# Kernel optimization log

Measured on AMD Instinct MI355X. Metric: run time of the kernel, lower is better.

The kernel has to match this reference:

```python
import jax, jax.numpy as jnp
import numpy as np

B, N, D, DE, E, L = 8, 4096, 128, 128, 262144, 2
FF = 4 * D  # feedforward hidden


def _ln(x, g, b, eps=1e-5):
    m = jnp.mean(x, axis=-1, keepdims=True)
    v = jnp.mean(jnp.square(x - m), axis=-1, keepdims=True)
    return (x - m) * jax.lax.rsqrt(v + eps) * g + b


def setup_inputs() -> dict:
    key = jax.random.key(0)
    ks = iter(jax.random.split(key, 40))

    def w(shape):
        fan_in = shape[-2]
        return jax.random.normal(next(ks), shape, jnp.float32) / np.sqrt(fan_in)

    return {
        "x": jax.random.normal(next(ks), (B, N, D), jnp.float32),
        "edge_index": jax.random.randint(next(ks), (2, E), 0, B * N, dtype=jnp.int32),
        "edge_attr": jax.random.normal(next(ks), (E, DE), jnp.float32),
        # message MLP (n_message = 3 linears)
        "msg_W0": w((L, 2 * D + DE, D)), "msg_b0": jnp.zeros((L, D)),
        "msg_W1": w((L, D, D)), "msg_b1": jnp.zeros((L, D)),
        "msg_W2": w((L, D, D)), "msg_b2": jnp.zeros((L, D)),
        "norm0_g": jnp.ones((L, D)), "norm0_b": jnp.zeros((L, D)),
        # feedforward
        "ff_W0": w((L, D, FF)), "ff_b0": jnp.zeros((L, FF)),
        "ff_W1": w((L, FF, D)), "ff_b1": jnp.zeros((L, D)),
        "norm1_g": jnp.ones((L, D)), "norm1_b": jnp.zeros((L, D)),
        # edge update MLP (n_edge_gvps = 3 linears)
        "edge_W0": w((L, 2 * D + DE, DE)), "edge_b0": jnp.zeros((L, DE)),
        "edge_W1": w((L, DE, DE)), "edge_b1": jnp.zeros((L, DE)),
        "edge_W2": w((L, DE, DE)), "edge_b2": jnp.zeros((L, DE)),
        "enorm_g": jnp.ones((L, DE)), "enorm_b": jnp.zeros((L, DE)),
    }


def reference(x, edge_index, edge_attr,
              msg_W0, msg_b0, msg_W1, msg_b1, msg_W2, msg_b2,
              norm0_g, norm0_b, ff_W0, ff_b0, ff_W1, ff_b1, norm1_g, norm1_b,
              edge_W0, edge_b0, edge_W1, edge_b1, edge_W2, edge_b2,
              enorm_g, enorm_b):
    Bx, Nx, Dx = x.shape
    n_nodes = Bx * Nx
    nodes = x.reshape(n_nodes, Dx)          # torch.flatten(x, 0, 1)
    src, dst = edge_index[0], edge_index[1]
    # in-degree for mean aggregation (guard isolated nodes)
    deg = jax.ops.segment_sum(jnp.ones((edge_attr.shape[0],), nodes.dtype), dst,
                              num_segments=n_nodes)
    inv_deg = (1.0 / jnp.maximum(deg, 1.0))[:, None]

    n_layers = msg_W0.shape[0]
    for l in range(n_layers):
        # --- node message passing (mean aggr at dst) ---
        h = jnp.concatenate([nodes[src], edge_attr, nodes[dst]], axis=-1)  # [E, 2D+DE]
        m = jax.nn.relu(h @ msg_W0[l] + msg_b0[l])
        m = jax.nn.relu(m @ msg_W1[l] + msg_b1[l])
        m = m @ msg_W2[l] + msg_b2[l]
        agg = jax.ops.segment_sum(m, dst, num_segments=n_nodes) * inv_deg
        nodes = _ln(nodes + agg, norm0_g[l], norm0_b[l])
        # --- feedforward ---
        ff = jax.nn.relu(nodes @ ff_W0[l] + ff_b0[l]) @ ff_W1[l] + ff_b1[l]
        nodes = _ln(nodes + ff, norm1_g[l], norm1_b[l])
        # --- edge update ---
        eh = jnp.concatenate([nodes[src], edge_attr, nodes[dst]], axis=-1)
        e = jax.nn.relu(eh @ edge_W0[l] + edge_b0[l])
        e = jax.nn.relu(e @ edge_W1[l] + edge_b1[l])
        e = e @ edge_W2[l] + edge_b2[l]
        edge_attr = _ln(edge_attr + e, enorm_g[l], enorm_b[l])

    return nodes.reshape(Bx, Nx, Dx)
```

## Files before the change

kernel.cpp:

```cpp
#include <hip/hip_runtime.h>

#define E_      262144
#define NNODES  32768
#define L_      2

typedef __attribute__((ext_vector_type(8))) short  bf16x8;
typedef __attribute__((ext_vector_type(4))) float  f32x4;

typedef __attribute__((address_space(1))) const unsigned int gu32;
typedef __attribute__((address_space(3))) unsigned int       lu32;

__device__ __forceinline__ void gl16(const void* g, void* l) {
    __builtin_amdgcn_global_load_lds((gu32*)g, (lu32*)l, 16, 0, 0);
}

__device__ __forceinline__ float bf2f(unsigned short u) {
    union { unsigned int i; float f; } v; v.i = ((unsigned int)u) << 16; return v.f;
}
__device__ __forceinline__ unsigned short f2bf(float f) {
    union { float f; unsigned int i; } v; v.f = f;
    unsigned int r = v.i + 0x7FFFu + ((v.i >> 16) & 1u);
    return (unsigned short)(r >> 16);
}

__global__ __launch_bounds__(256)
void k_cvt2(const float* __restrict__ a, unsigned short* __restrict__ oa, int n4a,
            const float* __restrict__ b, unsigned short* __restrict__ ob, int n4b)
{
    int i = blockIdx.x * 256 + threadIdx.x;
    if (i < n4a) {
        float4 v = reinterpret_cast<const float4*>(a)[i];
        ushort4 o; o.x = f2bf(v.x); o.y = f2bf(v.y); o.z = f2bf(v.z); o.w = f2bf(v.w);
        reinterpret_cast<ushort4*>(oa)[i] = o;
    } else if (i < n4a + n4b) {
        int j = i - n4a;
        float4 v = reinterpret_cast<const float4*>(b)[j];
        ushort4 o; o.x = f2bf(v.x); o.y = f2bf(v.y); o.z = f2bf(v.z); o.w = f2bf(v.w);
        reinterpret_cast<ushort4*>(ob)[j] = o;
    }
}

struct TD  { const float* s; unsigned short* d; int off; int K; int nsh; };
struct TDA { TD v[13]; int total; };

__global__ __launch_bounds__(256)
void k_transpose_all(TDA t)
{
    int idx = blockIdx.x * 256 + threadIdx.x;
    if (idx >= t.total) return;
    int j = 0;
#pragma unroll
    for (int m = 1; m < 13; ++m) if (idx >= t.v[m].off) j = m;
    const TD& td = t.v[j];
    int local = idx - td.off;
    int k = local >> td.nsh;
    int n = local & ((1 << td.nsh) - 1);
    td.d[(size_t)n * td.K + k] = f2bf(td.s[local]);
}

template<bool LNEPI>
__global__ __launch_bounds__(256, 4)
void fused_mlp3(const unsigned short* __restrict__ nodes,
                const unsigned short* __restrict__ eattr,
                const int*            __restrict__ ei,
                const unsigned short* __restrict__ W0T,
                const unsigned short* __restrict__ W1T,
                const unsigned short* __restrict__ W2T,
                const float* __restrict__ b0, const float* __restrict__ b1,
                const float* __restrict__ b2,
                const float* __restrict__ g,  const float* __restrict__ bb,
                unsigned short* __restrict__ out)
{
    __shared__ unsigned short S0[64 * 64];
    __shared__ unsigned short SB[128 * 64];
    __shared__ unsigned short H [64 * 128];

    const int tid  = threadIdx.x;
    const int lane = tid & 63;
    const int w    = tid >> 6;
    const int wr   = w >> 1, wc = w & 1;
    const int m0   = blockIdx.x * 64;

    const int lrow = lane >> 3;
    const int soff = ((lane & 7) ^ lrow) * 8;

    char* S0c = (char*)S0;
    char* SBc = (char*)SB;
    char* Hc  = (char*)H;

    const unsigned short *pS[2], *pD[2], *pE[2];
#pragma unroll
    for (int i = 0; i < 2; ++i) {
        int r = w * 16 + i * 8 + lrow;
        int e = m0 + r;
        pS[i] = nodes + (size_t)ei[e]      * 128 + soff;
        pD[i] = nodes + (size_t)ei[E_ + e] * 128 + soff;
        pE[i] = eattr + (size_t)e          * 128 + soff;
    }

    f32x4 acc[2][4];
    auto zacc = [&]() {
#pragma unroll
        for (int m = 0; m < 2; ++m)
#pragma unroll
            for (int n = 0; n < 4; ++n) acc[m][n] = (f32x4){0.f, 0.f, 0.f, 0.f};
    };

    auto mma = [&](const char* Ab, int abytes, int kbase) {
#pragma unroll
        for (int ks = 0; ks < 2; ++ks) {
            const int kb = (kbase + ks * 32) * 2 + (lane >> 4) * 16;
            bf16x8 a[2], b[4];
#pragma unroll
            for (int m = 0; m < 2; ++m) {
                int row = wr * 32 + m * 16 + (lane & 15);
                a[m] = *reinterpret_cast<const bf16x8*>(Ab + row * abytes + (kb ^ ((row & 7) << 4)));
            }
            const int kbb = ks * 64 + (lane >> 4) * 16;
#pragma unroll
            for (int n = 0; n < 4; ++n) {
                int row = wc * 64 + n * 16 + (lane & 15);
                b[n] = *reinterpret_cast<const bf16x8*>(SBc + row * 128 + (kbb ^ ((row & 7) << 4)));
            }
#pragma unroll
            for (int m = 0; m < 2; ++m)
#pragma unroll
                for (int n = 0; n < 4; ++n)
                    acc[m][n] = __builtin_amdgcn_mfma_f32_16x16x32_bf16(a[m], b[n], acc[m][n], 0, 0, 0);
        }
    };

    auto towrite = [&](const float* bias) {
#pragma unroll
        for (int n = 0; n < 4; ++n) {
            int cg = wc * 64 + n * 16 + (lane & 15);
            float bi = bias[cg];
#pragma unroll
            for (int m = 0; m < 2; ++m) {
#pragma unroll
                for (int j = 0; j < 4; ++j) {
                    int rg = wr * 32 + m * 16 + (lane >> 4) * 4 + j;
                    float v = fmaxf(acc[m][n][j] + bi, 0.f);
                    *(unsigned short*)(Hc + rg * 256 + ((2 * cg) ^ ((rg & 7) << 4))) = f2bf(v);
                }
            }
        }
    };

    zacc();
    for (int k0 = 0; k0 < 384; k0 += 64) {
#pragma unroll
        for (int i = 0; i < 2; ++i) {
            const unsigned short* pa = (k0 < 128 ? pS[i] : (k0 < 256 ? pE[i] : pD[i])) + (k0 & 64);
            gl16(pa, S0c + (w * 16 + i * 8) * 128);
        }
#pragma unroll
        for (int i = 0; i < 4; ++i)
            gl16(W0T + (size_t)(w * 32 + i * 8 + lrow) * 384 + k0 + soff,
                 SBc + (w * 32 + i * 8) * 128);
        __syncthreads();
        mma(S0c, 128, 0);
        __syncthreads();
    }
    towrite(b0);
    zacc();
#pragma unroll
    for (int k0 = 0; k0 < 128; k0 += 64) {
#pragma unroll
        for (int i = 0; i < 4; ++i)
            gl16(W1T + (size_t)(w * 32 + i * 8 + lrow) * 128 + k0 + soff,
                 SBc + (w * 32 + i * 8) * 128);
        __syncthreads();
        mma(Hc, 256, k0);
        __syncthreads();
    }
    towrite(b1);
    zacc();
#pragma unroll
    for (int k0 = 0; k0 < 128; k0 += 64) {
#pragma unroll
        for (int i = 0; i < 4; ++i)
            gl16(W2T + (size_t)(w * 32 + i * 8 + lrow) * 128 + k0 + soff,
                 SBc + (w * 32 + i * 8) * 128);
        __syncthreads();
        mma(Hc, 256, k0);
        __syncthreads();
    }

    if (!LNEPI) {
#pragma unroll
        for (int n = 0; n < 4; ++n) {
            int cg = wc * 64 + n * 16 + (lane & 15);
            float bi = b2[cg];
#pragma unroll
            for (int m = 0; m < 2; ++m) {
                int rg = m0 + wr * 32 + m * 16 + (lane >> 4) * 4;
                unsigned short* cp = out + (size_t)rg * 128 + cg;
#pragma unroll
                for (int j = 0; j < 4; ++j)
                    cp[(size_t)j * 128] = f2bf(acc[m][n][j] + bi);
            }
        }
    } else {
#pragma unroll
        for (int n = 0; n < 4; ++n) {
            int cg = wc * 64 + n * 16 + (lane & 15);
            float bi = b2[cg];
#pragma unroll
            for (int m = 0; m < 2; ++m) {
#pragma unroll
                for (int j = 0; j < 4; ++j) {
                    int rg = m0 + wr * 32 + m * 16 + (lane >> 4) * 4 + j;
                    acc[m][n][j] += bi + bf2f(eattr[(size_t)rg * 128 + cg]);
                }
            }
        }
        float* ps = (float*)SBc;
        float* pq = ps + 128;
#pragma unroll
        for (int m = 0; m < 2; ++m) {
#pragma unroll
            for (int j = 0; j < 4; ++j) {
                float s = 0.f, q = 0.f;
#pragma unroll
                for (int n = 0; n < 4; ++n) {
                    float v = acc[m][n][j];
                    s += v; q += v * v;
                }
#pragma unroll
                for (int msk = 1; msk < 16; msk <<= 1) {
                    s += __shfl_xor(s, msk);
                    q += __shfl_xor(q, msk);
                }
                if ((lane & 15) == 0) {
                    int rl = wr * 32 + m * 16 + (lane >> 4) * 4 + j;
                    ps[wc * 64 + rl] = s;
                    pq[wc * 64 + rl] = q;
                }
            }
        }
        __syncthreads();
#pragma unroll
        for (int m = 0; m < 2; ++m) {
#pragma unroll
            for (int j = 0; j < 4; ++j) {
                int rl = wr * 32 + m * 16 + (lane >> 4) * 4 + j;
                float S = ps[rl] + ps[64 + rl];
                float Q = pq[rl] + pq[64 + rl];
                float mean = S * (1.f / 128.f);
                float var  = Q * (1.f / 128.f) - mean * mean;
                float rs   = rsqrtf(var + 1e-5f);
                int rg = m0 + rl;
#pragma unroll
                for (int n = 0; n < 4; ++n) {
                    int cg = wc * 64 + n * 16 + (lane & 15);
                    out[(size_t)rg * 128 + cg] =
                        f2bf((acc[m][n][j] - mean) * rs * g[cg] + bb[cg]);
                }
            }
        }
    }
}

template<int BM, int K, int NTOT, bool RELU>
__global__ __launch_bounds__(256)
void mlp_gemm(const unsigned short* __restrict__ Abase,
              const unsigned short* __restrict__ WT,
              const float*          __restrict__ bias,
              unsigned short*       __restrict__ C)
{
    constexpr int MI = BM / 32;
    __shared__ unsigned short Alds[BM * 64];
    __shared__ unsigned short Blds[128 * 64];

    const int tid  = threadIdx.x;
    const int lane = tid & 63;
    const int w    = tid >> 6;
    const int wr   = w >> 1, wc = w & 1;
    const int m0   = blockIdx.x * BM;
    const int n0   = blockIdx.y * 128;

    const int lrow = lane >> 3;
    const int soff = ((lane & 7) ^ lrow) * 8;

    const unsigned short *pS[MI], *pB[4];
#pragma unroll
    for (int i = 0; i < MI; ++i)
        pS[i] = Abase + (size_t)(m0 + w * (BM / 4) + i * 8 + lrow) * K + soff;
#pragma unroll
    for (int i = 0; i < 4; ++i)
        pB[i] = WT + (size_t)(n0 + w * 32 + i * 8 + lrow) * K + soff;

    f32x4 acc[MI][4];
#pragma unroll
    for (int m = 0; m < MI; ++m)
#pragma unroll
        for (int n = 0; n < 4; ++n) acc[m][n] = (f32x4){0.f, 0.f, 0.f, 0.f};

#pragma unroll
    for (int k0 = 0; k0 < K; k0 += 64) {
#pragma unroll
        for (int i = 0; i < MI; ++i)
            gl16(pS[i] + k0, Alds + (w * (BM / 4) + i * 8) * 64);
#pragma unroll
        for (int i = 0; i < 4; ++i)
            gl16(pB[i] + k0, Blds + (w * 32 + i * 8) * 64);
        __syncthreads();

#pragma unroll
        for (int ks = 0; ks < 2; ++ks) {
            const int kb = ks * 64 + (lane >> 4) * 16;
            bf16x8 a[MI], b[4];
#pragma unroll
            for (int m = 0; m < MI; ++m) {
                int row = wr * (BM / 2) + m * 16 + (lane & 15);
                a[m] = *reinterpret_cast<const bf16x8*>(
                    (const char*)Alds + row * 128 + (kb ^ ((row & 7) << 4)));
            }
#pragma unroll
            for (int n = 0; n < 4; ++n) {
                int row = wc * 64 + n * 16 + (lane & 15);
                b[n] = *reinterpret_cast<const bf16x8*>(
                    (const char*)Blds + row * 128 + (kb ^ ((row & 7) << 4)));
            }
#pragma unroll
            for (int m = 0; m < MI; ++m)
#pragma unroll
                for (int n = 0; n < 4; ++n)
                    acc[m][n] = __builtin_amdgcn_mfma_f32_16x16x32_bf16(a[m], b[n], acc[m][n], 0, 0, 0);
        }
        __syncthreads();
    }

#pragma unroll
    for (int n = 0; n < 4; ++n) {
        int colg = n0 + wc * 64 + n * 16 + (lane & 15);
        float bi = bias[colg];
#pragma unroll
        for (int m = 0; m < MI; ++m) {
            int rowg = m0 + wr * (BM / 2) + m * 16 + (lane >> 4) * 4;
            unsigned short* cp = C + (size_t)rowg * NTOT + colg;
#pragma unroll
            for (int j = 0; j < 4; ++j) {
                float r = acc[m][n][j] + bi;
                if (RELU) r = fmaxf(r, 0.f);
                cp[(size_t)j * NTOT] = f2bf(r);
            }
        }
    }
}

__global__ __launch_bounds__(256)
void k_deg(const int* __restrict__ ei, int* __restrict__ deg)
{
    int e = blockIdx.x * 256 + threadIdx.x;
    atomicAdd(&deg[ei[E_ + e]], 1);
}

__global__ __launch_bounds__(1024)
void k_scan(const int* __restrict__ deg, int* __restrict__ off)
{
    __shared__ int part[1024];
    const int t = threadIdx.x;
    const int base = t * 32;
    int loc[32];
    int s = 0;
#pragma unroll
    for (int i = 0; i < 32; ++i) { loc[i] = s; s += deg[base + i]; }
    part[t] = s;
    __syncthreads();
    for (int d = 1; d < 1024; d <<= 1) {
        int v = (t >= d) ? part[t - d] : 0;
        __syncthreads();
        part[t] += v;
        __syncthreads();
    }
    const int pre = (t == 0) ? 0 : part[t - 1];
#pragma unroll
    for (int i = 0; i < 32; ++i) off[base + i] = pre + loc[i];
    if (t == 1023) off[NNODES] = pre + s;
}

__global__ __launch_bounds__(256)
void k_bucket(const int* __restrict__ ei, int* __restrict__ cursor, int* __restrict__ elist)
{
    int e = blockIdx.x * 256 + threadIdx.x;
    int d = ei[E_ + e];
    int pos = atomicAdd(&cursor[d], 1);
    elist[pos] = e;
}

__global__ __launch_bounds__(256)
void k_aggln(const unsigned short* __restrict__ m,
             const int* __restrict__ off, const int* __restrict__ elist,
             const unsigned short* __restrict__ nodes_in,
             const float* __restrict__ g, const float* __restrict__ bb,
             unsigned short* __restrict__ nodes_out)
{
    const int v    = blockIdx.x * 4 + (threadIdx.x >> 6);
    const int lane = threadIdx.x & 63;
    const int c    = lane * 2;
    const int beg  = off[v], end = off[v + 1];

    float a0 = 0.f, a1 = 0.f;
    for (int i = beg; i < end; ++i) {
        int e = elist[i];
        unsigned int u = *reinterpret_cast<const unsigned int*>(m + (size_t)e * 128 + c);
        a0 += bf2f((unsigned short)(u & 0xffffu));
        a1 += bf2f((unsigned short)(u >> 16));
    }
    const float inv = 1.f / fmaxf((float)(end - beg), 1.f);
    const size_t o = (size_t)v * 128 + c;
    float x0 = bf2f(nodes_in[o])     + a0 * inv;
    float x1 = bf2f(nodes_in[o + 1]) + a1 * inv;

    float s = x0 + x1, sq = x0 * x0 + x1 * x1;
#pragma unroll
    for (int mm = 1; mm < 64; mm <<= 1) { s += __shfl_xor(s, mm); sq += __shfl_xor(sq, mm); }
    float mean = s * (1.f / 128.f);
    float var  = sq * (1.f / 128.f) - mean * mean;
    float rs   = rsqrtf(var + 1e-5f);
    nodes_out[o]     = f2bf((x0 - mean) * rs * g[c]     + bb[c]);
    nodes_out[o + 1] = f2bf((x1 - mean) * rs * g[c + 1] + bb[c + 1]);
}

template<bool F32OUT>
__global__ __launch_bounds__(256)
void k_ln(const unsigned short* __restrict__ base,
          const unsigned short* __restrict__ res,
          const float* __restrict__ g, const float* __restrict__ bb,
          void* __restrict__ outp)
{
    int row  = blockIdx.x * 4 + (threadIdx.x >> 6);
    int lane = threadIdx.x & 63;
    int c    = lane * 2;
    size_t off = (size_t)row * 128 + c;

    float x0 = bf2f(base[off])     + bf2f(res[off]);
    float x1 = bf2f(base[off + 1]) + bf2f(res[off + 1]);
    float s = x0 + x1, sq = x0 * x0 + x1 * x1;
#pragma unroll
    for (int m = 1; m < 64; m <<= 1) { s += __shfl_xor(s, m); sq += __shfl_xor(sq, m); }
    float mean = s * (1.f / 128.f);
    float var  = sq * (1.f / 128.f) - mean * mean;
    float rs   = rsqrtf(var + 1e-5f);
    float y0 = (x0 - mean) * rs * g[c]     + bb[c];
    float y1 = (x1 - mean) * rs * g[c + 1] + bb[c + 1];
    if (F32OUT) {
        ((float*)outp)[off]     = y0;
        ((float*)outp)[off + 1] = y1;
    } else {
        ((unsigned short*)outp)[off]     = f2bf(y0);
        ((unsigned short*)outp)[off + 1] = f2bf(y1);
    }
}

extern "C" void kernel_launch(void* const* d_in, const int* in_sizes, int n_in,
                              void* d_out, int out_size, void* d_ws, size_t ws_size,
                              hipStream_t stream)
{
    const float* x      = (const float*)d_in[0];
    const int*   ei     = (const int*)d_in[1];
    const float* eat0   = (const float*)d_in[2];
    const float* msg_W0 = (const float*)d_in[3];
    const float* msg_b0 = (const float*)d_in[4];
    const float* msg_W1 = (const float*)d_in[5];
    const float* msg_b1 = (const float*)d_in[6];
    const float* msg_W2 = (const float*)d_in[7];
    const float* msg_b2 = (const float*)d_in[8];
    const float* n0g    = (const float*)d_in[9];
    const float* n0b    = (const float*)d_in[10];
    const float* ff_W0  = (const float*)d_in[11];
    const float* ff_b0  = (const float*)d_in[12];
    const float* ff_W1  = (const float*)d_in[13];
    const float* ff_b1  = (const float*)d_in[14];
    const float* n1g    = (const float*)d_in[15];
    const float* n1b    = (const float*)d_in[16];
    const float* e_W0   = (const float*)d_in[17];
    const float* e_b0   = (const float*)d_in[18];
    const float* e_W1   = (const float*)d_in[19];
    const float* e_b1   = (const float*)d_in[20];
    const float* e_W2   = (const float*)d_in[21];
    const float* e_b2   = (const float*)d_in[22];
    const float* eng    = (const float*)d_in[23];
    const float* enb    = (const float*)d_in[24];

    char* ws = (char*)d_ws;
    const size_t MB = (size_t)1 << 20;
    unsigned short* nodes = (unsigned short*)(ws);
    unsigned short* edgec = (unsigned short*)(ws + 8 * MB);
    unsigned short* tmpA  = (unsigned short*)(ws + 72 * MB);
    unsigned short* ffh   = (unsigned short*)(ws + 136 * MB);
    unsigned short* ffo   = tmpA;
    unsigned short* wt    = (unsigned short*)(ws + 200 * MB);
    int*            deg   = (int*)(ws + 202 * MB);
    int*            off   = (int*)(ws + 202 * MB + 256 * 1024);
    int*            cur   = (int*)(ws + 202 * MB + 512 * 1024);
    int*            elist = (int*)(ws + 202 * MB + 768 * 1024);

    unsigned short* p = wt;
    unsigned short *wt_m0[L_], *wt_m1[L_], *wt_m2[L_], *wt_f0[L_], *wt_f1[L_];
    for (int l = 0; l < L_; ++l) {
        wt_m0[l] = p; p += 384 * 128;
        wt_m1[l] = p; p += 128 * 128;
        wt_m2[l] = p; p += 128 * 128;
        wt_f0[l] = p; p += 128 * 512;
        wt_f1[l] = p; p += 512 * 128;
    }
    unsigned short* wt_e0 = p; p += 384 * 128;
    unsigned short* wt_e1 = p; p += 128 * 128;
    unsigned short* wt_e2 = p; p += 128 * 128;

    TDA tda; int toff = 0, ti = 0;
    auto addT = [&](const float* s, unsigned short* d, int K, int N) {
        tda.v[ti++] = TD{s, d, toff, K, (N == 512 ? 9 : 7)};
        toff += K * N;
    };
    for (int l = 0; l < L_; ++l) {
        addT(msg_W0 + l * 384 * 128, wt_m0[l], 384, 128);
        addT(msg_W1 + l * 128 * 128, wt_m1[l], 128, 128);
        addT(msg_W2 + l * 128 * 128, wt_m2[l], 128, 128);
        addT(ff_W0  + l * 128 * 512, wt_f0[l], 128, 512);
        addT(ff_W1  + l * 512 * 128, wt_f1[l], 512, 128);
    }
    addT(e_W0, wt_e0, 384, 128);
    addT(e_W1, wt_e1, 128, 128);
    addT(e_W2, wt_e2, 128, 128);
    tda.total = toff;
    k_transpose_all<<<(toff + 255) / 256, 256, 0, stream>>>(tda);

    const int n4a = NNODES * 128 / 4, n4b = E_ * 128 / 4;
    k_cvt2<<<(n4a + n4b + 255) / 256, 256, 0, stream>>>(x, nodes, n4a, eat0, edgec, n4b);

    hipMemsetAsync(deg, 0, NNODES * sizeof(int), stream);
    k_deg<<<E_ / 256, 256, 0, stream>>>(ei, deg);
    k_scan<<<1, 1024, 0, stream>>>(deg, off);
    hipMemcpyAsync(cur, off, NNODES * sizeof(int), hipMemcpyDeviceToDevice, stream);
    k_bucket<<<E_ / 256, 256, 0, stream>>>(ei, cur, elist);

    const dim3 gE(E_ / 64, 1), gN64(NNODES / 64, 1), gF0(NNODES / 128, 4);

    for (int l = 0; l < L_; ++l) {
        fused_mlp3<false><<<gE, 256, 0, stream>>>(nodes, edgec, ei,
            wt_m0[l], wt_m1[l], wt_m2[l],
            msg_b0 + l * 128, msg_b1 + l * 128, msg_b2 + l * 128,
            nullptr, nullptr, tmpA);
        k_aggln<<<NNODES / 4, 256, 0, stream>>>(tmpA, off, elist, nodes,
            n0g + l * 128, n0b + l * 128, nodes);
        mlp_gemm<128, 128, 512, true ><<<gF0, 256, 0, stream>>>(nodes, wt_f0[l], ff_b0 + l * 512, ffh);
        mlp_gemm<64,  512, 128, false><<<gN64, 256, 0, stream>>>(ffh, wt_f1[l], ff_b1 + l * 128, ffo);
        if (l == L_ - 1) {
            k_ln<true ><<<NNODES / 4, 256, 0, stream>>>(nodes, ffo, n1g + l * 128, n1b + l * 128, d_out);
        } else {
            k_ln<false><<<NNODES / 4, 256, 0, stream>>>(nodes, ffo, n1g + l * 128, n1b + l * 128, nodes);
        }
        if (l == 0) {
            fused_mlp3<true><<<gE, 256, 0, stream>>>(nodes, edgec, ei,
                wt_e0, wt_e1, wt_e2, e_b0, e_b1, e_b2, eng, enb, edgec);
        }
    }
}
```

Measured before the change: 462.8 us.

## Double-buffer LDS staging in fused edge MLP with 32-wide K tiles

Splits the shared-memory staging buffers for the gathered edge inputs and the weight tiles into two halves with a 32-element K step. The next tile's global-to-LDS loads are issued before the MFMAs on the current tile, so gather latency overlaps compute and one barrier per step is dropped. In exchange there are twice as many K steps, each with less MFMA work to hide latency behind, and a new XOR swizzle for the 64-byte rows that could bring back bank conflicts.

```diff
diff --git a/kernel.cpp b/kernel.cpp
--- a/kernel.cpp
+++ b/kernel.cpp
@@ -71,8 +71,8 @@
                 const float* __restrict__ g,  const float* __restrict__ bb,
                 unsigned short* __restrict__ out)
 {
-    __shared__ unsigned short S0[64 * 64];
-    __shared__ unsigned short SB[128 * 64];
+    __shared__ unsigned short S0[2][64 * 32];
+    __shared__ unsigned short SB[2][128 * 32];
     __shared__ unsigned short H [64 * 128];
 
     const int tid  = threadIdx.x;
@@ -81,22 +81,17 @@
     const int wr   = w >> 1, wc = w & 1;
     const int m0   = blockIdx.x * 64;
 
-    const int lrow = lane >> 3;
-    const int soff = ((lane & 7) ^ lrow) * 8;
+    const int l4   = lane >> 2;
+    const int soff = (((lane & 3) ^ ((l4 >> 1) & 3)) << 3);
 
     char* S0c = (char*)S0;
     char* SBc = (char*)SB;
     char* Hc  = (char*)H;
 
-    const unsigned short *pS[2], *pD[2], *pE[2];
-#pragma unroll
-    for (int i = 0; i < 2; ++i) {
-        int r = w * 16 + i * 8 + lrow;
-        int e = m0 + r;
-        pS[i] = nodes + (size_t)ei[e]      * 128 + soff;
-        pD[i] = nodes + (size_t)ei[E_ + e] * 128 + soff;
-        pE[i] = eattr + (size_t)e          * 128 + soff;
-    }
+    const int er = m0 + w * 16 + l4;
+    const unsigned short* pS = nodes + (size_t)ei[er]      * 128 + soff;
+    const unsigned short* pD = nodes + (size_t)ei[E_ + er] * 128 + soff;
+    const unsigned short* pE = eattr + (size_t)er          * 128 + soff;
 
     f32x4 acc[2][4];
     auto zacc = [&]() {
@@ -106,28 +101,58 @@
             for (int n = 0; n < 4; ++n) acc[m][n] = (f32x4){0.f, 0.f, 0.f, 0.f};
     };
 
-    auto mma = [&](const char* Ab, int abytes, int kbase) {
-#pragma unroll
-        for (int ks = 0; ks < 2; ++ks) {
-            const int kb = (kbase + ks * 32) * 2 + (lane >> 4) * 16;
-            bf16x8 a[2], b[4];
-#pragma unroll
-            for (int m = 0; m < 2; ++m) {
-                int row = wr * 32 + m * 16 + (lane & 15);
-                a[m] = *reinterpret_cast<const bf16x8*>(Ab + row * abytes + (kb ^ ((row & 7) << 4)));
-            }
-            const int kbb = ks * 64 + (lane >> 4) * 16;
-#pragma unroll
-            for (int n = 0; n < 4; ++n) {
-                int row = wc * 64 + n * 16 + (lane & 15);
-                b[n] = *reinterpret_cast<const bf16x8*>(SBc + row * 128 + (kbb ^ ((row & 7) << 4)));
-            }
-#pragma unroll
-            for (int m = 0; m < 2; ++m)
-#pragma unroll
-                for (int n = 0; n < 4; ++n)
-                    acc[m][n] = __builtin_amdgcn_mfma_f32_16x16x32_bf16(a[m], b[n], acc[m][n], 0, 0, 0);
-        }
+    auto stageA = [&](int t, int buf) {
+        const unsigned short* p = (t < 4 ? pS : (t < 8 ? pE : pD)) + (t & 3) * 32;
+        gl16(p, S0c + buf * 4096 + w * 1024);
+    };
+    auto stageW = [&](const unsigned short* WT, int Kr, int t, int buf) {
+#pragma unroll
+        for (int i = 0; i < 2; ++i)
+            gl16(WT + (size_t)(w * 32 + i * 16 + l4) * Kr + t * 32 + soff,
+                 SBc + buf * 8192 + w * 2048 + i * 1024);
+    };
+
+    const int q4 = (lane >> 4) << 4;
+
+    auto ldB = [&](int buf, bf16x8* b) {
+#pragma unroll
+        for (int n = 0; n < 4; ++n) {
+            int row = wc * 64 + n * 16 + (lane & 15);
+            b[n] = *reinterpret_cast<const bf16x8*>(
+                SBc + buf * 8192 + row * 64 + (q4 ^ (((row >> 1) & 3) << 4)));
+        }
+    };
+
+    auto mmaP1 = [&](int buf) {
+        bf16x8 a[2], b[4];
+        ldB(buf, b);
+#pragma unroll
+        for (int m = 0; m < 2; ++m) {
+            int row = wr * 32 + m * 16 + (lane & 15);
+            a[m] = *reinterpret_cast<const bf16x8*>(
+                S0c + buf * 4096 + row * 64 + (q4 ^ (((row >> 1) & 3) << 4)));
+        }
+#pragma unroll
+        for (int m = 0; m < 2; ++m)
+#pragma unroll
+            for (int n = 0; n < 4; ++n)
+                acc[m][n] = __builtin_amdgcn_mfma_f32_16x16x32_bf16(a[m], b[n], acc[m][n], 0, 0, 0);
+    };
+
+    auto mmaH = [&](int t, int buf) {
+        bf16x8 a[2], b[4];
+        ldB(buf, b);
+#pragma unroll
+        for (int m = 0; m < 2; ++m) {
+            int row = wr * 32 + m * 16 + (lane & 15);
+            a[m] = *reinterpret_cast<const bf16x8*>(
+                Hc + row * 256 + ((t * 64 + q4) ^ ((row & 7) << 4)));
+        }
+#pragma unroll
+        for (int m = 0; m < 2; ++m)
+#pragma unroll
+            for (int n = 0; n < 4; ++n)
+                acc[m][n] = __builtin_amdgcn_mfma_f32_16x16x32_bf16(a[m], b[n], acc[m][n], 0, 0, 0);
     };
 
     auto towrite = [&](const float* bias) {
@@ -148,43 +173,39 @@
     };
 
     zacc();
-    for (int k0 = 0; k0 < 384; k0 += 64) {
-#pragma unroll
-        for (int i = 0; i < 2; ++i) {
-            const unsigned short* pa = (k0 < 128 ? pS[i] : (k0 < 256 ? pE[i] : pD[i])) + (k0 & 64);
-            gl16(pa, S0c + (w * 16 + i * 8) * 128);
-        }
-#pragma unroll
-        for (int i = 0; i < 4; ++i)
-            gl16(W0T + (size_t)(w * 32 + i * 8 + lrow) * 384 + k0 + soff,
-                 SBc + (w * 32 + i * 8) * 128);
-        __syncthreads();
-        mma(S0c, 128, 0);
-        __syncthreads();
+    stageA(0, 0); stageW(W0T, 384, 0, 0);
+    __syncthreads();
+    int pb = 0;
+#pragma unroll
+    for (int t = 0; t < 12; ++t) {
+        if (t < 11) { stageA(t + 1, pb ^ 1); stageW(W0T, 384, t + 1, pb ^ 1); }
+        mmaP1(pb);
+        __syncthreads();
+        pb ^= 1;
     }
     towrite(b0);
     zacc();
-#pragma unroll
-    for (int k0 = 0; k0 < 128; k0 += 64) {
-#pragma unroll
-        for (int i = 0; i < 4; ++i)
-            gl16(W1T + (size_t)(w * 32 + i * 8 + lrow) * 128 + k0 + soff,
-                 SBc + (w * 32 + i * 8) * 128);
-        __syncthreads();
-        mma(Hc, 256, k0);
-        __syncthreads();
+    stageW(W1T, 128, 0, 0);
+    __syncthreads();
+    pb = 0;
+#pragma unroll
+    for (int t = 0; t < 4; ++t) {
+        if (t < 3) stageW(W1T, 128, t + 1, pb ^ 1);
+        mmaH(t, pb);
+        __syncthreads();
+        pb ^= 1;
     }
     towrite(b1);
     zacc();
-#pragma unroll
-    for (int k0 = 0; k0 < 128; k0 += 64) {
-#pragma unroll
-        for (int i = 0; i < 4; ++i)
-            gl16(W2T + (size_t)(w * 32 + i * 8 + lrow) * 128 + k0 + soff,
-                 SBc + (w * 32 + i * 8) * 128);
-        __syncthreads();
-        mma(Hc, 256, k0);
-        __syncthreads();
+    stageW(W2T, 128, 0, 0);
+    __syncthreads();
+    pb = 0;
+#pragma unroll
+    for (int t = 0; t < 4; ++t) {
+        if (t < 3) stageW(W2T, 128, t + 1, pb ^ 1);
+        mmaH(t, pb);
+        __syncthreads();
+        pb ^= 1;
     }
 
     if (!LNEPI) {
```

Measured after the change: 490.3 us. 5.9% more time.

## Precompute per-node first-layer projections instead of per-edge gathered GEMM

Applied to the files above, without the earlier changes.

The first linear layer of the message and edge MLPs is split by linearity: the source and destination node blocks are multiplied once per node in a new pq_gemm kernel, which writes fp32 P and Q tables. The per-edge kernel then runs only the edge-attribute part of the first GEMM (K=128 instead of 384) and adds the gathered P[src] and Q[dst] rows before the ReLU. This removes two thirds of the per-edge first-layer MFMA work and the bf16 node-row gathers. In exchange it adds a node-level GEMM launch and gathers of fp32 rows (1 KB per edge), which changes the memory traffic pattern and the rounding.

```diff
diff --git a/kernel.cpp b/kernel.cpp
--- a/kernel.cpp
+++ b/kernel.cpp
@@ -41,7 +41,7 @@
 }
 
 struct TD  { const float* s; unsigned short* d; int off; int K; int nsh; };
-struct TDA { TD v[13]; int total; };
+struct TDA { TD v[19]; int total; };
 
 __global__ __launch_bounds__(256)
 void k_transpose_all(TDA t)
@@ -50,7 +50,7 @@
     if (idx >= t.total) return;
     int j = 0;
 #pragma unroll
-    for (int m = 1; m < 13; ++m) if (idx >= t.v[m].off) j = m;
+    for (int m = 1; m < 19; ++m) if (idx >= t.v[m].off) j = m;
     const TD& td = t.v[j];
     int local = idx - td.off;
     int k = local >> td.nsh;
@@ -58,45 +58,117 @@
     td.d[(size_t)n * td.K + k] = f2bf(td.s[local]);
 }
 
-template<bool LNEPI>
-__global__ __launch_bounds__(256, 4)
-void fused_mlp3(const unsigned short* __restrict__ nodes,
-                const unsigned short* __restrict__ eattr,
-                const int*            __restrict__ ei,
-                const unsigned short* __restrict__ W0T,
-                const unsigned short* __restrict__ W1T,
-                const unsigned short* __restrict__ W2T,
-                const float* __restrict__ b0, const float* __restrict__ b1,
-                const float* __restrict__ b2,
-                const float* __restrict__ g,  const float* __restrict__ bb,
-                unsigned short* __restrict__ out)
-{
-    __shared__ unsigned short S0[64 * 64];
-    __shared__ unsigned short SB[128 * 64];
-    __shared__ unsigned short H [64 * 128];
+__global__ __launch_bounds__(256)
+void pq_gemm(const unsigned short* __restrict__ A,
+             const unsigned short* __restrict__ WT,
+             const float* __restrict__ b0,
+             float* __restrict__ PQ)
+{
+    __shared__ unsigned short Alds[64 * 64];
+    __shared__ unsigned short Blds[128 * 64];
 
     const int tid  = threadIdx.x;
     const int lane = tid & 63;
     const int w    = tid >> 6;
     const int wr   = w >> 1, wc = w & 1;
     const int m0   = blockIdx.x * 64;
+    const int n0   = blockIdx.y * 128;
 
     const int lrow = lane >> 3;
     const int soff = ((lane & 7) ^ lrow) * 8;
 
-    char* S0c = (char*)S0;
-    char* SBc = (char*)SB;
-    char* Hc  = (char*)H;
-
-    const unsigned short *pS[2], *pD[2], *pE[2];
-#pragma unroll
-    for (int i = 0; i < 2; ++i) {
-        int r = w * 16 + i * 8 + lrow;
-        int e = m0 + r;
-        pS[i] = nodes + (size_t)ei[e]      * 128 + soff;
-        pD[i] = nodes + (size_t)ei[E_ + e] * 128 + soff;
-        pE[i] = eattr + (size_t)e          * 128 + soff;
-    }
+    char* Ac = (char*)Alds; char* Bc = (char*)Blds;
+
+    const unsigned short *pS[2], *pB[4];
+#pragma unroll
+    for (int i = 0; i < 2; ++i)
+        pS[i] = A + (size_t)(m0 + w * 16 + i * 8 + lrow) * 128 + soff;
+#pragma unroll
+    for (int i = 0; i < 4; ++i)
+        pB[i] = WT + (size_t)(n0 + w * 32 + i * 8 + lrow) * 128 + soff;
+
+    f32x4 acc[2][4];
+#pragma unroll
+    for (int m = 0; m < 2; ++m)
+#pragma unroll
+        for (int n = 0; n < 4; ++n) acc[m][n] = (f32x4){0.f, 0.f, 0.f, 0.f};
+
+#pragma unroll
+    for (int k0 = 0; k0 < 128; k0 += 64) {
+#pragma unroll
+        for (int i = 0; i < 2; ++i) gl16(pS[i] + k0, Ac + (w * 16 + i * 8) * 128);
+#pragma unroll
+        for (int i = 0; i < 4; ++i) gl16(pB[i] + k0, Bc + (w * 32 + i * 8) * 128);
+        __syncthreads();
+#pragma unroll
+        for (int ks = 0; ks < 2; ++ks) {
+            const int kb = ks * 64 + (lane >> 4) * 16;
+            bf16x8 a[2], b[4];
+#pragma unroll
+            for (int m = 0; m < 2; ++m) {
+                int row = wr * 32 + m * 16 + (lane & 15);
+                a[m] = *reinterpret_cast<const bf16x8*>(Ac + row * 128 + (kb ^ ((row & 7) << 4)));
+            }
+#pragma unroll
+            for (int n = 0; n < 4; ++n) {
+                int row = wc * 64 + n * 16 + (lane & 15);
+                b[n] = *reinterpret_cast<const bf16x8*>(Bc + row * 128 + (kb ^ ((row & 7) << 4)));
+            }
+#pragma unroll
+            for (int m = 0; m < 2; ++m)
+#pragma unroll
+                for (int n = 0; n < 4; ++n)
+                    acc[m][n] = __builtin_amdgcn_mfma_f32_16x16x32_bf16(a[m], b[n], acc[m][n], 0, 0, 0);
+        }
+        __syncthreads();
+    }
+
+#pragma unroll
+    for (int n = 0; n < 4; ++n) {
+        int colg = n0 + wc * 64 + n * 16 + (lane & 15);
+        float bi = (colg < 128) ? b0[colg] : 0.f;
+#pragma unroll
+        for (int m = 0; m < 2; ++m) {
+            int rowg = m0 + wr * 32 + m * 16 + (lane >> 4) * 4;
+            float* cp = PQ + (size_t)rowg * 256 + colg;
+#pragma unroll
+            for (int j = 0; j < 4; ++j)
+                cp[(size_t)j * 256] = acc[m][n][j] + bi;
+        }
+    }
+}
+
+template<bool LNEPI>
+__global__ __launch_bounds__(256, 4)
+void fused_mlp3(const unsigned short* __restrict__ ein,
+                const float*          __restrict__ PQ,
+                const int*            __restrict__ ei,
+                const unsigned short* __restrict__ W0bT,
+                const unsigned short* __restrict__ W1T,
+                const unsigned short* __restrict__ W2T,
+                const float* __restrict__ b1, const float* __restrict__ b2,
+                const float* __restrict__ g,  const float* __restrict__ bb,
+                unsigned short* __restrict__ out)
+{
+    __shared__ unsigned short S0[64 * 64];
+    __shared__ unsigned short SB[128 * 64];
+    __shared__ unsigned short H [64 * 128];
+
+    const int tid  = threadIdx.x;
+    const int lane = tid & 63;
+    const int w    = tid >> 6;
+    const int wr   = w >> 1, wc = w & 1;
+    const int m0   = blockIdx.x * 64;
+
+    const int lrow = lane >> 3;
+    const int soff = ((lane & 7) ^ lrow) * 8;
+
+    char* S0c = (char*)S0; char* SBc = (char*)SB; char* Hc = (char*)H;
+
+    const unsigned short* pA[2];
+#pragma unroll
+    for (int i = 0; i < 2; ++i)
+        pA[i] = ein + (size_t)(m0 + w * 16 + i * 8 + lrow) * 128 + soff;
 
     f32x4 acc[2][4];
     auto zacc = [&]() {
@@ -106,21 +178,34 @@
             for (int n = 0; n < 4; ++n) acc[m][n] = (f32x4){0.f, 0.f, 0.f, 0.f};
     };
 
-    auto mma = [&](const char* Ab, int abytes, int kbase) {
+    auto stageA = [&](int k0) {
+#pragma unroll
+        for (int i = 0; i < 2; ++i)
+            gl16(pA[i] + k0, S0c + (w * 16 + i * 8) * 128);
+    };
+    auto stageW = [&](const unsigned short* WT, int k0) {
+#pragma unroll
+        for (int i = 0; i < 4; ++i)
+            gl16(WT + (size_t)(w * 32 + i * 8 + lrow) * 128 + k0 + soff,
+                 SBc + (w * 32 + i * 8) * 128);
+    };
+
+    auto mma = [&](const char* Ab, int abytes, int kb0) {
 #pragma unroll
         for (int ks = 0; ks < 2; ++ks) {
-            const int kb = (kbase + ks * 32) * 2 + (lane >> 4) * 16;
+            const int kb = ks * 64 + (lane >> 4) * 16;
             bf16x8 a[2], b[4];
 #pragma unroll
             for (int m = 0; m < 2; ++m) {
                 int row = wr * 32 + m * 16 + (lane & 15);
-                a[m] = *reinterpret_cast<const bf16x8*>(Ab + row * abytes + (kb ^ ((row & 7) << 4)));
-            }
-            const int kbb = ks * 64 + (lane >> 4) * 16;
+                a[m] = *reinterpret_cast<const bf16x8*>(
+                    Ab + row * abytes + ((kb0 + kb) ^ ((row & 7) << 4)));
+            }
 #pragma unroll
             for (int n = 0; n < 4; ++n) {
                 int row = wc * 64 + n * 16 + (lane & 15);
-                b[n] = *reinterpret_cast<const bf16x8*>(SBc + row * 128 + (kbb ^ ((row & 7) << 4)));
+                b[n] = *reinterpret_cast<const bf16x8*>(
+                    SBc + row * 128 + (kb ^ ((row & 7) << 4)));
             }
 #pragma unroll
             for (int m = 0; m < 2; ++m)
@@ -130,60 +215,77 @@
         }
     };
 
-    auto towrite = [&](const float* bias) {
+    auto towrite = [&](const float* bias, bool relu) {
 #pragma unroll
         for (int n = 0; n < 4; ++n) {
             int cg = wc * 64 + n * 16 + (lane & 15);
-            float bi = bias[cg];
+            float bi = bias ? bias[cg] : 0.f;
 #pragma unroll
             for (int m = 0; m < 2; ++m) {
 #pragma unroll
                 for (int j = 0; j < 4; ++j) {
                     int rg = wr * 32 + m * 16 + (lane >> 4) * 4 + j;
-                    float v = fmaxf(acc[m][n][j] + bi, 0.f);
+                    float v = acc[m][n][j] + bi;
+                    if (relu) v = fmaxf(v, 0.f);
                     *(unsigned short*)(Hc + rg * 256 + ((2 * cg) ^ ((rg & 7) << 4))) = f2bf(v);
                 }
             }
         }
     };
 
+    auto pq_pass = [&]() {
+        const int r  = tid >> 2;
+        const int c0 = (tid & 3) * 32;
+        const int sv = ei[m0 + r], dv = ei[E_ + m0 + r];
+        const float* Pp = PQ + (size_t)sv * 256 + c0;
+        const float* Qp = PQ + (size_t)dv * 256 + 128 + c0;
+#pragma unroll
+        for (int i = 0; i < 4; ++i) {
+            char* hp = Hc + r * 256 + (((c0 + i * 8) * 2) ^ ((r & 7) << 4));
+            bf16x8 hv = *reinterpret_cast<bf16x8*>(hp);
+            float4 p0 = *reinterpret_cast<const float4*>(Pp + i * 8);
+            float4 p1 = *reinterpret_cast<const float4*>(Pp + i * 8 + 4);
+            float4 q0 = *reinterpret_cast<const float4*>(Qp + i * 8);
+            float4 q1 = *reinterpret_cast<const float4*>(Qp + i * 8 + 4);
+            bf16x8 o;
+            o[0] = (short)f2bf(fmaxf(bf2f((unsigned short)hv[0]) + p0.x + q0.x, 0.f));
+            o[1] = (short)f2bf(fmaxf(bf2f((unsigned short)hv[1]) + p0.y + q0.y, 0.f));
+            o[2] = (short)f2bf(fmaxf(bf2f((unsigned short)hv[2]) + p0.z + q0.z, 0.f));
+            o[3] = (short)f2bf(fmaxf(bf2f((unsigned short)hv[3]) + p0.w + q0.w, 0.f));
+            o[4] = (short)f2bf(fmaxf(bf2f((unsigned short)hv[4]) + p1.x + q1.x, 0.f));
+            o[5] = (short)f2bf(fmaxf(bf2f((unsigned short)hv[5]) + p1.y + q1.y, 0.f));
+            o[6] = (short)f2bf(fmaxf(bf2f((unsigned short)hv[6]) + p1.z + q1.z, 0.f));
+            o[7] = (short)f2bf(fmaxf(bf2f((unsigned short)hv[7]) + p1.w + q1.w, 0.f));
+            *reinterpret_cast<bf16x8*>(hp) = o;
+        }
+    };
+
     zacc();
-    for (int k0 = 0; k0 < 384; k0 += 64) {
-#pragma unroll
-        for (int i = 0; i < 2; ++i) {
-            const unsigned short* pa = (k0 < 128 ? pS[i] : (k0 < 256 ? pE[i] : pD[i])) + (k0 & 64);
-            gl16(pa, S0c + (w * 16 + i * 8) * 128);
-        }
-#pragma unroll
-        for (int i = 0; i < 4; ++i)
-            gl16(W0T + (size_t)(w * 32 + i * 8 + lrow) * 384 + k0 + soff,
-                 SBc + (w * 32 + i * 8) * 128);
+#pragma unroll
+    for (int t = 0; t < 2; ++t) {
+        stageA(t * 64); stageW(W0bT, t * 64);
         __syncthreads();
         mma(S0c, 128, 0);
         __syncthreads();
     }
-    towrite(b0);
+    towrite(nullptr, false);
+    __syncthreads();
+    pq_pass();
     zacc();
 #pragma unroll
-    for (int k0 = 0; k0 < 128; k0 += 64) {
-#pragma unroll
-        for (int i = 0; i < 4; ++i)
-            gl16(W1T + (size_t)(w * 32 + i * 8 + lrow) * 128 + k0 + soff,
-                 SBc + (w * 32 + i * 8) * 128);
-        __syncthreads();
-        mma(Hc, 256, k0);
-        __syncthreads();
-    }
-    towrite(b1);
+    for (int t = 0; t < 2; ++t) {
+        stageW(W1T, t * 64);
+        __syncthreads();
+        mma(Hc, 256, t * 128);
+        __syncthreads();
+    }
+    towrite(b1, true);
     zacc();
 #pragma unroll
-    for (int k0 = 0; k0 < 128; k0 += 64) {
-#pragma unroll
-        for (int i = 0; i < 4; ++i)
-            gl16(W2T + (size_t)(w * 32 + i * 8 + lrow) * 128 + k0 + soff,
-                 SBc + (w * 32 + i * 8) * 128);
-        __syncthreads();
-        mma(Hc, 256, k0);
+    for (int t = 0; t < 2; ++t) {
+        stageW(W2T, t * 64);
+        __syncthreads();
+        mma(Hc, 256, t * 128);
         __syncthreads();
     }
 
@@ -211,7 +313,7 @@
 #pragma unroll
                 for (int j = 0; j < 4; ++j) {
                     int rg = m0 + wr * 32 + m * 16 + (lane >> 4) * 4 + j;
-                    acc[m][n][j] += bi + bf2f(eattr[(size_t)rg * 128 + cg]);
+                    acc[m][n][j] += bi + bf2f(ein[(size_t)rg * 128 + cg]);
                 }
             }
         }
@@ -491,6 +593,7 @@
     unsigned short* edgec = (unsigned short*)(ws + 8 * MB);
     unsigned short* tmpA  = (unsigned short*)(ws + 72 * MB);
     unsigned short* ffh   = (unsigned short*)(ws + 136 * MB);
+    float*          PQ    = (float*)(ws + 168 * MB);
     unsigned short* ffo   = tmpA;
     unsigned short* wt    = (unsigned short*)(ws + 200 * MB);
     int*            deg   = (int*)(ws + 202 * MB);
@@ -499,17 +602,19 @@
     int*            elist = (int*)(ws + 202 * MB + 768 * 1024);
 
     unsigned short* p = wt;
-    unsigned short *wt_m0[L_], *wt_m1[L_], *wt_m2[L_], *wt_f0[L_], *wt_f1[L_];
+    unsigned short *wt_mac[L_], *wt_mb[L_], *wt_m1[L_], *wt_m2[L_], *wt_f0[L_], *wt_f1[L_];
     for (int l = 0; l < L_; ++l) {
-        wt_m0[l] = p; p += 384 * 128;
-        wt_m1[l] = p; p += 128 * 128;
-        wt_m2[l] = p; p += 128 * 128;
-        wt_f0[l] = p; p += 128 * 512;
-        wt_f1[l] = p; p += 512 * 128;
-    }
-    unsigned short* wt_e0 = p; p += 384 * 128;
-    unsigned short* wt_e1 = p; p += 128 * 128;
-    unsigned short* wt_e2 = p; p += 128 * 128;
+        wt_mac[l] = p; p += 256 * 128;
+        wt_mb[l]  = p; p += 128 * 128;
+        wt_m1[l]  = p; p += 128 * 128;
+        wt_m2[l]  = p; p += 128 * 128;
+        wt_f0[l]  = p; p += 128 * 512;
+        wt_f1[l]  = p; p += 512 * 128;
+    }
+    unsigned short* wt_eac = p; p += 256 * 128;
+    unsigned short* wt_eb  = p; p += 128 * 128;
+    unsigned short* wt_e1  = p; p += 128 * 128;
+    unsigned short* wt_e2  = p; p += 128 * 128;
 
     TDA tda; int toff = 0, ti = 0;
     auto addT = [&](const float* s, unsigned short* d, int K, int N) {
@@ -517,13 +622,18 @@
         toff += K * N;
     };
     for (int l = 0; l < L_; ++l) {
-        addT(msg_W0 + l * 384 * 128, wt_m0[l], 384, 128);
+        const float* W0 = msg_W0 + l * 384 * 128;
+        addT(W0,             wt_mac[l],         128, 128);
+        addT(W0 + 256 * 128, wt_mac[l] + 16384, 128, 128);
+        addT(W0 + 128 * 128, wt_mb[l],          128, 128);
         addT(msg_W1 + l * 128 * 128, wt_m1[l], 128, 128);
         addT(msg_W2 + l * 128 * 128, wt_m2[l], 128, 128);
         addT(ff_W0  + l * 128 * 512, wt_f0[l], 128, 512);
         addT(ff_W1  + l * 512 * 128, wt_f1[l], 512, 128);
     }
-    addT(e_W0, wt_e0, 384, 128);
+    addT(e_W0,             wt_eac,         128, 128);
+    addT(e_W0 + 256 * 128, wt_eac + 16384, 128, 128);
+    addT(e_W0 + 128 * 128, wt_eb,          128, 128);
     addT(e_W1, wt_e1, 128, 128);
     addT(e_W2, wt_e2, 128, 128);
     tda.total = toff;
@@ -538,13 +648,13 @@
     hipMemcpyAsync(cur, off, NNODES * sizeof(int), hipMemcpyDeviceToDevice, stream);
     k_bucket<<<E_ / 256, 256, 0, stream>>>(ei, cur, elist);
 
-    const dim3 gE(E_ / 64, 1), gN64(NNODES / 64, 1), gF0(NNODES / 128, 4);
+    const dim3 gE(E_ / 64, 1), gPQ(NNODES / 64, 2), gN64(NNODES / 64, 1), gF0(NNODES / 128, 4);
 
     for (int l = 0; l < L_; ++l) {
-        fused_mlp3<false><<<gE, 256, 0, stream>>>(nodes, edgec, ei,
-            wt_m0[l], wt_m1[l], wt_m2[l],
-            msg_b0 + l * 128, msg_b1 + l * 128, msg_b2 + l * 128,
-            nullptr, nullptr, tmpA);
+        pq_gemm<<<gPQ, 256, 0, stream>>>(nodes, wt_mac[l], msg_b0 + l * 128, PQ);
+        fused_mlp3<false><<<gE, 256, 0, stream>>>(edgec, PQ, ei,
+            wt_mb[l], wt_m1[l], wt_m2[l],
+            msg_b1 + l * 128, msg_b2 + l * 128, nullptr, nullptr, tmpA);
         k_aggln<<<NNODES / 4, 256, 0, stream>>>(tmpA, off, elist, nodes,
             n0g + l * 128, n0b + l * 128, nodes);
         mlp_gemm<128, 128, 512, true ><<<gF0, 256, 0, stream>>>(nodes, wt_f0[l], ff_b0 + l * 512, ffh);
@@ -555,8 +665,9 @@
             k_ln<false><<<NNODES / 4, 256, 0, stream>>>(nodes, ffo, n1g + l * 128, n1b + l * 128, nodes);
         }
         if (l == 0) {
-            fused_mlp3<true><<<gE, 256, 0, stream>>>(nodes, edgec, ei,
-                wt_e0, wt_e1, wt_e2, e_b0, e_b1, e_b2, eng, enb, edgec);
-        }
-    }
-}
+            pq_gemm<<<gPQ, 256, 0, stream>>>(nodes, wt_eac, e_b0, PQ);
+            fused_mlp3<true><<<gE, 256, 0, stream>>>(edgec, PQ, ei,
+                wt_eb, wt_e1, wt_e2, e_b1, e_b2, eng, enb, edgec);
+        }
+    }
+}
```

Result: slower. 588.0 us (+27.0%).

## Load MFMA operands directly from global memory instead of staging through LDS

Applied to the files above, without the earlier changes.

The fused edge MLP and the feedforward GEMMs now read A and B fragments for each MFMA straight from global memory into registers, dropping the global_load_lds staging buffers and most of the block barriers. The edge kernel keeps only the hidden-activation tile in LDS and reuses it for the layernorm reduction scratch. The goal is to remove LDS traffic and barrier stalls and to cut shared-memory use so more blocks fit per CU. The cost is redundant global and L2 reads, since each wave re-fetches weight rows with no LDS reuse, and less latency hiding for the gathered node rows. The feedforward first GEMM also moves from 128-row to 64-row tiles.

```diff
diff --git a/kernel.cpp b/kernel.cpp
--- a/kernel.cpp
+++ b/kernel.cpp
@@ -6,13 +6,6 @@
 
 typedef __attribute__((ext_vector_type(8))) short  bf16x8;
 typedef __attribute__((ext_vector_type(4))) float  f32x4;
-
-typedef __attribute__((address_space(1))) const unsigned int gu32;
-typedef __attribute__((address_space(3))) unsigned int       lu32;
-
-__device__ __forceinline__ void gl16(const void* g, void* l) {
-    __builtin_amdgcn_global_load_lds((gu32*)g, (lu32*)l, 16, 0, 0);
-}
 
 __device__ __forceinline__ float bf2f(unsigned short u) {
     union { unsigned int i; float f; } v; v.i = ((unsigned int)u) << 16; return v.f;
@@ -71,32 +64,25 @@
                 const float* __restrict__ g,  const float* __restrict__ bb,
                 unsigned short* __restrict__ out)
 {
-    __shared__ unsigned short S0[64 * 64];
-    __shared__ unsigned short SB[128 * 64];
-    __shared__ unsigned short H [64 * 128];
-
-    const int tid  = threadIdx.x;
-    const int lane = tid & 63;
-    const int w    = tid >> 6;
+    __shared__ unsigned short H[64 * 128];
+    char* Hc = (char*)H;
+
+    const int lane = threadIdx.x & 63;
+    const int w    = threadIdx.x >> 6;
     const int wr   = w >> 1, wc = w & 1;
     const int m0   = blockIdx.x * 64;
-
-    const int lrow = lane >> 3;
-    const int soff = ((lane & 7) ^ lrow) * 8;
-
-    char* S0c = (char*)S0;
-    char* SBc = (char*)SB;
-    char* Hc  = (char*)H;
-
-    const unsigned short *pS[2], *pD[2], *pE[2];
-#pragma unroll
-    for (int i = 0; i < 2; ++i) {
-        int r = w * 16 + i * 8 + lrow;
-        int e = m0 + r;
-        pS[i] = nodes + (size_t)ei[e]      * 128 + soff;
-        pD[i] = nodes + (size_t)ei[E_ + e] * 128 + soff;
-        pE[i] = eattr + (size_t)e          * 128 + soff;
-    }
+    const int koff = (lane >> 4) * 8;
+    const int arow = lane & 15;
+
+    const unsigned short *pAs[2], *pAe[2], *pAd[2];
+#pragma unroll
+    for (int m = 0; m < 2; ++m) {
+        int e = m0 + wr * 32 + m * 16 + arow;
+        pAs[m] = nodes + (size_t)ei[e]      * 128 + koff;
+        pAd[m] = nodes + (size_t)ei[E_ + e] * 128 + koff;
+        pAe[m] = eattr + (size_t)e          * 128 + koff;
+    }
+    const size_t brow = wc * 64 + (lane & 15);
 
     f32x4 acc[2][4];
     auto zacc = [&]() {
@@ -104,30 +90,6 @@
         for (int m = 0; m < 2; ++m)
 #pragma unroll
             for (int n = 0; n < 4; ++n) acc[m][n] = (f32x4){0.f, 0.f, 0.f, 0.f};
-    };
-
-    auto mma = [&](const char* Ab, int abytes, int kbase) {
-#pragma unroll
-        for (int ks = 0; ks < 2; ++ks) {
-            const int kb = (kbase + ks * 32) * 2 + (lane >> 4) * 16;
-            bf16x8 a[2], b[4];
-#pragma unroll
-            for (int m = 0; m < 2; ++m) {
-                int row = wr * 32 + m * 16 + (lane & 15);
-                a[m] = *reinterpret_cast<const bf16x8*>(Ab + row * abytes + (kb ^ ((row & 7) << 4)));
-            }
-            const int kbb = ks * 64 + (lane >> 4) * 16;
-#pragma unroll
-            for (int n = 0; n < 4; ++n) {
-                int row = wc * 64 + n * 16 + (lane & 15);
-                b[n] = *reinterpret_cast<const bf16x8*>(SBc + row * 128 + (kbb ^ ((row & 7) << 4)));
-            }
-#pragma unroll
-            for (int m = 0; m < 2; ++m)
-#pragma unroll
-                for (int n = 0; n < 4; ++n)
-                    acc[m][n] = __builtin_amdgcn_mfma_f32_16x16x32_bf16(a[m], b[n], acc[m][n], 0, 0, 0);
-        }
     };
 
     auto towrite = [&](const float* bias) {
@@ -147,45 +109,55 @@
         }
     };
 
+    auto phaseH = [&](const unsigned short* WT) {
+        zacc();
+#pragma unroll
+        for (int ks = 0; ks < 4; ++ks) {
+            bf16x8 a[2], b[4];
+#pragma unroll
+            for (int m = 0; m < 2; ++m) {
+                int row = wr * 32 + m * 16 + arow;
+                a[m] = *reinterpret_cast<const bf16x8*>(
+                    Hc + row * 256 + ((ks * 64 + (lane >> 4) * 16) ^ ((row & 7) << 4)));
+            }
+#pragma unroll
+            for (int n = 0; n < 4; ++n)
+                b[n] = *reinterpret_cast<const bf16x8*>(
+                    WT + (brow + n * 16) * 128 + koff + ks * 32);
+#pragma unroll
+            for (int m = 0; m < 2; ++m)
+#pragma unroll
+                for (int n = 0; n < 4; ++n)
+                    acc[m][n] = __builtin_amdgcn_mfma_f32_16x16x32_bf16(a[m], b[n], acc[m][n], 0, 0, 0);
+        }
+    };
+
     zacc();
-    for (int k0 = 0; k0 < 384; k0 += 64) {
-#pragma unroll
-        for (int i = 0; i < 2; ++i) {
-            const unsigned short* pa = (k0 < 128 ? pS[i] : (k0 < 256 ? pE[i] : pD[i])) + (k0 & 64);
-            gl16(pa, S0c + (w * 16 + i * 8) * 128);
-        }
-#pragma unroll
-        for (int i = 0; i < 4; ++i)
-            gl16(W0T + (size_t)(w * 32 + i * 8 + lrow) * 384 + k0 + soff,
-                 SBc + (w * 32 + i * 8) * 128);
-        __syncthreads();
-        mma(S0c, 128, 0);
-        __syncthreads();
+#pragma unroll
+    for (int ks = 0; ks < 12; ++ks) {
+        bf16x8 a[2], b[4];
+#pragma unroll
+        for (int m = 0; m < 2; ++m) {
+            const unsigned short* p = (ks < 4 ? pAs[m] : (ks < 8 ? pAe[m] : pAd[m]));
+            a[m] = *reinterpret_cast<const bf16x8*>(p + (ks & 3) * 32);
+        }
+#pragma unroll
+        for (int n = 0; n < 4; ++n)
+            b[n] = *reinterpret_cast<const bf16x8*>(
+                W0T + (brow + n * 16) * 384 + koff + ks * 32);
+#pragma unroll
+        for (int m = 0; m < 2; ++m)
+#pragma unroll
+            for (int n = 0; n < 4; ++n)
+                acc[m][n] = __builtin_amdgcn_mfma_f32_16x16x32_bf16(a[m], b[n], acc[m][n], 0, 0, 0);
     }
     towrite(b0);
-    zacc();
-#pragma unroll
-    for (int k0 = 0; k0 < 128; k0 += 64) {
-#pragma unroll
-        for (int i = 0; i < 4; ++i)
-            gl16(W1T + (size_t)(w * 32 + i * 8 + lrow) * 128 + k0 + soff,
-                 SBc + (w * 32 + i * 8) * 128);
-        __syncthreads();
-        mma(Hc, 256, k0);
-        __syncthreads();
-    }
+    __syncthreads();
+    phaseH(W1T);
+    __syncthreads();
     towrite(b1);
-    zacc();
-#pragma unroll
-    for (int k0 = 0; k0 < 128; k0 += 64) {
-#pragma unroll
-        for (int i = 0; i < 4; ++i)
-            gl16(W2T + (size_t)(w * 32 + i * 8 + lrow) * 128 + k0 + soff,
-                 SBc + (w * 32 + i * 8) * 128);
-        __syncthreads();
-        mma(Hc, 256, k0);
-        __syncthreads();
-    }
+    __syncthreads();
+    phaseH(W2T);
 
     if (!LNEPI) {
 #pragma unroll
@@ -215,7 +187,8 @@
                 }
             }
         }
-        float* ps = (float*)SBc;
+        __syncthreads();
+        float* ps = (float*)Hc;
         float* pq = ps + 128;
 #pragma unroll
         for (int m = 0; m < 2; ++m) {
@@ -262,74 +235,48 @@
     }
 }
 
-template<int BM, int K, int NTOT, bool RELU>
-__global__ __launch_bounds__(256)
-void mlp_gemm(const unsigned short* __restrict__ Abase,
-              const unsigned short* __restrict__ WT,
-              const float*          __restrict__ bias,
-              unsigned short*       __restrict__ C)
-{
-    constexpr int MI = BM / 32;
-    __shared__ unsigned short Alds[BM * 64];
-    __shared__ unsigned short Blds[128 * 64];
-
-    const int tid  = threadIdx.x;
-    const int lane = tid & 63;
-    const int w    = tid >> 6;
+template<int K, int NTOT, bool RELU>
+__global__ __launch_bounds__(256, 4)
+void mlp_gemm_direct(const unsigned short* __restrict__ A,
+                     const unsigned short* __restrict__ WT,
+                     const float* __restrict__ bias,
+                     unsigned short* __restrict__ C)
+{
+    const int lane = threadIdx.x & 63;
+    const int w    = threadIdx.x >> 6;
     const int wr   = w >> 1, wc = w & 1;
-    const int m0   = blockIdx.x * BM;
+    const int m0   = blockIdx.x * 64;
     const int n0   = blockIdx.y * 128;
-
-    const int lrow = lane >> 3;
-    const int soff = ((lane & 7) ^ lrow) * 8;
-
-    const unsigned short *pS[MI], *pB[4];
-#pragma unroll
-    for (int i = 0; i < MI; ++i)
-        pS[i] = Abase + (size_t)(m0 + w * (BM / 4) + i * 8 + lrow) * K + soff;
-#pragma unroll
-    for (int i = 0; i < 4; ++i)
-        pB[i] = WT + (size_t)(n0 + w * 32 + i * 8 + lrow) * K + soff;
-
-    f32x4 acc[MI][4];
-#pragma unroll
-    for (int m = 0; m < MI; ++m)
+    const int koff = (lane >> 4) * 8;
+
+    const unsigned short *pA[2], *pB[4];
+#pragma unroll
+    for (int m = 0; m < 2; ++m)
+        pA[m] = A + (size_t)(m0 + wr * 32 + m * 16 + (lane & 15)) * K + koff;
+#pragma unroll
+    for (int n = 0; n < 4; ++n)
+        pB[n] = WT + (size_t)(n0 + wc * 64 + n * 16 + (lane & 15)) * K + koff;
+
+    f32x4 acc[2][4];
+#pragma unroll
+    for (int m = 0; m < 2; ++m)
 #pragma unroll
         for (int n = 0; n < 4; ++n) acc[m][n] = (f32x4){0.f, 0.f, 0.f, 0.f};
 
 #pragma unroll
-    for (int k0 = 0; k0 < K; k0 += 64) {
-#pragma unroll
-        for (int i = 0; i < MI; ++i)
-            gl16(pS[i] + k0, Alds + (w * (BM / 4) + i * 8) * 64);
-#pragma unroll
-        for (int i = 0; i < 4; ++i)
-            gl16(pB[i] + k0, Blds + (w * 32 + i * 8) * 64);
-        __syncthreads();
-
-#pragma unroll
-        for (int ks = 0; ks < 2; ++ks) {
-            const int kb = ks * 64 + (lane >> 4) * 16;
-            bf16x8 a[MI], b[4];
-#pragma unroll
-            for (int m = 0; m < MI; ++m) {
-                int row = wr * (BM / 2) + m * 16 + (lane & 15);
-                a[m] = *reinterpret_cast<const bf16x8*>(
-                    (const char*)Alds + row * 128 + (kb ^ ((row & 7) << 4)));
-            }
-#pragma unroll
-            for (int n = 0; n < 4; ++n) {
-                int row = wc * 64 + n * 16 + (lane & 15);
-                b[n] = *reinterpret_cast<const bf16x8*>(
-                    (const char*)Blds + row * 128 + (kb ^ ((row & 7) << 4)));
-            }
-#pragma unroll
-            for (int m = 0; m < MI; ++m)
-#pragma unroll
-                for (int n = 0; n < 4; ++n)
-                    acc[m][n] = __builtin_amdgcn_mfma_f32_16x16x32_bf16(a[m], b[n], acc[m][n], 0, 0, 0);
-        }
-        __syncthreads();
+    for (int ks = 0; ks < K / 32; ++ks) {
+        bf16x8 a[2], b[4];
+#pragma unroll
+        for (int m = 0; m < 2; ++m)
+            a[m] = *reinterpret_cast<const bf16x8*>(pA[m] + ks * 32);
+#pragma unroll
+        for (int n = 0; n < 4; ++n)
+            b[n] = *reinterpret_cast<const bf16x8*>(pB[n] + ks * 32);
+#pragma unroll
+        for (int m = 0; m < 2; ++m)
+#pragma unroll
+            for (int n = 0; n < 4; ++n)
+                acc[m][n] = __builtin_amdgcn_mfma_f32_16x16x32_bf16(a[m], b[n], acc[m][n], 0, 0, 0);
     }
 
 #pragma unroll
@@ -337,8 +284,8 @@
         int colg = n0 + wc * 64 + n * 16 + (lane & 15);
         float bi = bias[colg];
 #pragma unroll
-        for (int m = 0; m < MI; ++m) {
-            int rowg = m0 + wr * (BM / 2) + m * 16 + (lane >> 4) * 4;
+        for (int m = 0; m < 2; ++m) {
+            int rowg = m0 + wr * 32 + m * 16 + (lane >> 4) * 4;
             unsigned short* cp = C + (size_t)rowg * NTOT + colg;
 #pragma unroll
             for (int j = 0; j < 4; ++j) {
@@ -538,7 +485,7 @@
     hipMemcpyAsync(cur, off, NNODES * sizeof(int), hipMemcpyDeviceToDevice, stream);
     k_bucket<<<E_ / 256, 256, 0, stream>>>(ei, cur, elist);
 
-    const dim3 gE(E_ / 64, 1), gN64(NNODES / 64, 1), gF0(NNODES / 128, 4);
+    const dim3 gE(E_ / 64, 1), gN64(NNODES / 64, 1), gF0(NNODES / 64, 4);
 
     for (int l = 0; l < L_; ++l) {
         fused_mlp3<false><<<gE, 256, 0, stream>>>(nodes, edgec, ei,
@@ -547,8 +494,8 @@
             nullptr, nullptr, tmpA);
         k_aggln<<<NNODES / 4, 256, 0, stream>>>(tmpA, off, elist, nodes,
             n0g + l * 128, n0b + l * 128, nodes);
-        mlp_gemm<128, 128, 512, true ><<<gF0, 256, 0, stream>>>(nodes, wt_f0[l], ff_b0 + l * 512, ffh);
-        mlp_gemm<64,  512, 128, false><<<gN64, 256, 0, stream>>>(ffh, wt_f1[l], ff_b1 + l * 128, ffo);
+        mlp_gemm_direct<128, 512, true ><<<gF0, 256, 0, stream>>>(nodes, wt_f0[l], ff_b0 + l * 512, ffh);
+        mlp_gemm_direct<512, 128, false><<<gN64, 256, 0, stream>>>(ffh, wt_f1[l], ff_b1 + l * 128, ffo);
         if (l == L_ - 1) {
             k_ln<true ><<<NNODES / 4, 256, 0, stream>>>(nodes, ffo, n1g + l * 128, n1b + l * 128, d_out);
         } else {
```

After: 878.3 us. 89.8% more time.
